# Kernel optimization log

Measured on AMD Instinct MI355X. Metric: run time of the kernel, lower is better.

The kernel has to match this reference:

```python
import jax, jax.numpy as jnp
import numpy as np

VOCAB, E, H = 10000, 128, 256
B, K = 32768, 8


def setup_inputs() -> dict:
    key = jax.random.key(0)
    ks = jax.random.split(key, 14)
    s_in = 1.0 / np.sqrt(E + H)
    return {
        "x": jax.random.randint(ks[0], (1, B), 0, VOCAB),
        "h_pre": jax.random.normal(ks[1], (B, H), jnp.float32),
        "c_pre": jax.random.normal(ks[2], (B, H), jnp.float32),
        "child_cells": jax.random.normal(ks[3], (K, B, H), jnp.float32),
        "child_weights": jax.random.normal(ks[4], (K, B, H), jnp.float32),
        "embed_table": jax.random.normal(ks[5], (VOCAB, E), jnp.float32) * 0.02,
        "Wf": jax.random.normal(ks[6], (H, E + H), jnp.float32) * s_in,
        "bf": jnp.zeros((H,), jnp.float32),
        "Wi": jax.random.normal(ks[7], (H, E + H), jnp.float32) * s_in,
        "bi": jnp.zeros((H,), jnp.float32),
        "Wo": jax.random.normal(ks[8], (H, E + H), jnp.float32) * s_in,
        "bo": jnp.zeros((H,), jnp.float32),
        "Wc": jax.random.normal(ks[9], (H, E + H), jnp.float32) * s_in,
        "bc": jnp.zeros((H,), jnp.float32),
    }


def reference(x, h_pre, c_pre, child_cells, child_weights, embed_table,
              Wf, bf, Wi, bi, Wo, bo, Wc, bc):
    emb = embed_table[x[0]]                      # [B, E]  (squeeze(0))
    xh = jnp.concatenate([emb, h_pre], axis=1)   # [B, E+H] shared concat
    f = jax.nn.sigmoid(xh @ Wf.T + bf)           # [B, H]
    i = jax.nn.sigmoid(xh @ Wi.T + bi)
    c_ = jnp.tanh(xh @ Wc.T + bc)
    # tree-LSTM branch: softmax over [own candidate + K children] along axis 0
    all_cells = jnp.concatenate([c_[None], child_cells], axis=0)      # [K+1,B,H]
    all_w = jnp.concatenate([i[None], child_weights], axis=0)         # [K+1,B,H]
    w = jax.nn.softmax(all_w, axis=0)
    c_cur = jnp.sum(w * all_cells, axis=0)       # [B, H]
    o = jax.nn.sigmoid(xh @ Wo.T + bo)
    h_cur = o * jnp.tanh(c_cur)
    return (h_cur, c_cur)
```

## Files before the change

### kernel.cpp

```cpp
#include <hip/hip_runtime.h>

#define B_SZ   32768
#define H_SZ   256
#define E_SZ   128
#define K_CH   8
#define XH_K   384
#define N_G    768

typedef __attribute__((ext_vector_type(8))) short  short8;
typedef __attribute__((ext_vector_type(4))) short  s16x4;
typedef __attribute__((ext_vector_type(4))) float  f32x4;

static __device__ __forceinline__ short f2bf(float f) {
  union { float f; unsigned u; } v; v.f = f;
  unsigned u = v.u;
  return (short)((u + 0x7fffu + ((u >> 16) & 1u)) >> 16);
}

static __device__ __forceinline__ float bf2f(short s) {
  union { unsigned u; float f; } v;
  v.u = ((unsigned)(unsigned short)s) << 16;
  return v.f;
}

static __device__ __forceinline__ float sigmoid_f(float x) {
  return 1.0f / (1.0f + __expf(-x));
}

static __device__ __forceinline__ float tanh_f(float x) {
  float xc = fminf(fmaxf(x, -40.0f), 40.0f);
  float e  = __expf(2.0f * xc);
  return (e - 1.0f) / (e + 1.0f);
}

static __device__ __forceinline__ f32x4 exp4(f32x4 x) {
  f32x4 r;
#pragma unroll
  for (int c = 0; c < 4; ++c) r[c] = __expf(x[c]);
  return r;
}

static __device__ __forceinline__ void gload_lds16(const short* g, short* l) {
  __builtin_amdgcn_global_load_lds(
      (const __attribute__((address_space(1))) unsigned int*)g,
      (__attribute__((address_space(3))) unsigned int*)l, 16, 0, 0);
}

__global__ __launch_bounds__(256) void prep_xh(const int* __restrict__ x,
                                               const float* __restrict__ h_pre,
                                               const float* __restrict__ emb,
                                               short* __restrict__ xh) {
  int t = blockIdx.x * 256 + threadIdx.x;
  int b = t / 96;
  int c = (t - b * 96) * 4;
  f32x4 v;
  if (c < E_SZ) {
    int row = x[b];
    v = *(const f32x4*)(emb + (size_t)row * E_SZ + c);
  } else {
    v = *(const f32x4*)(h_pre + (size_t)b * H_SZ + (c - E_SZ));
  }
  s16x4 o;
#pragma unroll
  for (int i = 0; i < 4; ++i) o[i] = f2bf(v[i]);
  *(s16x4*)(xh + (size_t)b * XH_K + c) = o;
}

__global__ __launch_bounds__(256) void prep_w(const float* __restrict__ Wi,
                                              const float* __restrict__ Wo,
                                              const float* __restrict__ Wc,
                                              short* __restrict__ Wcat) {
  int t = blockIdx.x * 256 + threadIdx.x;
  int n = t / 96;
  int c = (t - n * 96) * 4;
  const float* src = (n < H_SZ)     ? (Wi + (size_t)n * XH_K)
                   : (n < 2 * H_SZ) ? (Wo + (size_t)(n - H_SZ) * XH_K)
                                    : (Wc + (size_t)(n - 2 * H_SZ) * XH_K);
  f32x4 v = *(const f32x4*)(src + c);
  s16x4 o;
#pragma unroll
  for (int i = 0; i < 4; ++i) o[i] = f2bf(v[i]);
  *(s16x4*)(Wcat + (size_t)n * XH_K + c) = o;
}

__global__ __launch_bounds__(256) void gemm_gates(const short* __restrict__ xh,
                                                  const short* __restrict__ Wcat,
                                                  const float* __restrict__ bi,
                                                  const float* __restrict__ bo,
                                                  const float* __restrict__ bc,
                                                  short* __restrict__ gates) {
  __shared__ short As[128 * 32];
  __shared__ short Bs[128 * 32];

  const int wave = threadIdx.x >> 6;
  const int lane = threadIdx.x & 63;
  const int ln = lane & 15;
  const int q  = lane >> 4;
  const int m0 = blockIdx.y * 128 + (wave >> 1) * 64;
  const int n0 = blockIdx.x * 128 + (wave & 1) * 64;
  const int Am = blockIdx.y * 128;
  const int Bn = blockIdx.x * 128;

  f32x4 acc[4][4] = {};

  for (int ks = 0; ks < 12; ++ks) {
    if (ks) __syncthreads();
#pragma unroll
    for (int s = 0; s < 2; ++s) {
      const int segb = s * 256 + wave * 64;
      const int seg  = segb + lane;
      const int row  = seg >> 2;
      const int ch8  = (seg & 3) * 8;
      gload_lds16(xh   + (size_t)(Am + row) * XH_K + ks * 32 + ch8, &As[segb * 8]);
      gload_lds16(Wcat + (size_t)(Bn + row) * XH_K + ks * 32 + ch8, &Bs[segb * 8]);
    }
    __syncthreads();

    short8 a[4], b[4];
    const int mw = (wave >> 1) * 64;
    const int nw = (wave & 1) * 64;
#pragma unroll
    for (int i = 0; i < 4; ++i)
      a[i] = *(const short8*)&As[(mw + i * 16 + ln) * 32 + q * 8];
#pragma unroll
    for (int j = 0; j < 4; ++j)
      b[j] = *(const short8*)&Bs[(nw + j * 16 + ln) * 32 + q * 8];
#pragma unroll
    for (int i = 0; i < 4; ++i)
#pragma unroll
      for (int j = 0; j < 4; ++j)
        acc[i][j] = __builtin_amdgcn_mfma_f32_16x16x32_bf16(a[i], b[j], acc[i][j], 0, 0, 0);
  }

#pragma unroll
  for (int j = 0; j < 4; ++j) {
    const int col  = n0 + j * 16 + ln;
    const int gate = col >> 8;
    const int cc   = col & 255;
    const float bias = (gate == 0) ? bi[cc] : (gate == 1) ? bo[cc] : bc[cc];
#pragma unroll
    for (int i = 0; i < 4; ++i) {
#pragma unroll
      for (int r = 0; r < 4; ++r) {
        const int row = m0 + i * 16 + q * 4 + r;
        float v = acc[i][j][r] + bias;
        v = (gate == 2) ? tanh_f(v) : sigmoid_f(v);
        gates[(size_t)row * N_G + col] = f2bf(v);
      }
    }
  }
}

__global__ __launch_bounds__(256, 4) void combine(const short* __restrict__ gates,
                                                  const float* __restrict__ ccells,
                                                  const float* __restrict__ cweights,
                                                  float* __restrict__ out) {
  int t = blockIdx.x * 256 + threadIdx.x;
  int b = t >> 5;
  int h = (t & 31) * 8;
  const short* grow = gates + (size_t)b * N_G;

  s16x4 i0 = *(const s16x4*)(grow + h);
  s16x4 i1 = *(const s16x4*)(grow + h + 4);
  s16x4 o0 = *(const s16x4*)(grow + H_SZ + h);
  s16x4 o1 = *(const s16x4*)(grow + H_SZ + h + 4);
  s16x4 c0 = *(const s16x4*)(grow + 2 * H_SZ + h);
  s16x4 c1 = *(const s16x4*)(grow + 2 * H_SZ + h + 4);

  f32x4 iv0, iv1, cv0, cv1;
#pragma unroll
  for (int c = 0; c < 4; ++c) {
    iv0[c] = bf2f(i0[c]); iv1[c] = bf2f(i1[c]);
    cv0[c] = bf2f(c0[c]); cv1[c] = bf2f(c1[c]);
  }

  f32x4 e0 = exp4(iv0), e1 = exp4(iv1);
  f32x4 num0 = e0 * cv0, num1 = e1 * cv1;
  f32x4 den0 = e0,       den1 = e1;

#pragma unroll
  for (int k = 0; k < K_CH; ++k) {
    size_t off = ((size_t)k * B_SZ + b) * H_SZ + h;
    f32x4 w0 = *(const f32x4*)(cweights + off);
    f32x4 w1 = *(const f32x4*)(cweights + off + 4);
    f32x4 l0 = *(const f32x4*)(ccells + off);
    f32x4 l1 = *(const f32x4*)(ccells + off + 4);
    f32x4 x0 = exp4(w0), x1 = exp4(w1);
    num0 += x0 * l0;  den0 += x0;
    num1 += x1 * l1;  den1 += x1;
  }

  f32x4 hv0, hv1, cc0, cc1;
#pragma unroll
  for (int c = 0; c < 4; ++c) {
    cc0[c] = num0[c] / den0[c];
    cc1[c] = num1[c] / den1[c];
    hv0[c] = bf2f(o0[c]) * tanh_f(cc0[c]);
    hv1[c] = bf2f(o1[c]) * tanh_f(cc1[c]);
  }
  float* oh = out + (size_t)b * H_SZ + h;
  float* oc = out + (size_t)B_SZ * H_SZ + (size_t)b * H_SZ + h;
  *(f32x4*)oh = hv0;  *(f32x4*)(oh + 4) = hv1;
  *(f32x4*)oc = cc0;  *(f32x4*)(oc + 4) = cc1;
}

extern "C" void kernel_launch(void* const* d_in, const int* in_sizes, int n_in,
                              void* d_out, int out_size, void* d_ws, size_t ws_size,
                              hipStream_t stream) {
  const int*   x             = (const int*)d_in[0];
  const float* h_pre         = (const float*)d_in[1];
  const float* child_cells   = (const float*)d_in[3];
  const float* child_weights = (const float*)d_in[4];
  const float* emb           = (const float*)d_in[5];
  const float* Wi            = (const float*)d_in[8];
  const float* bi            = (const float*)d_in[9];
  const float* Wo            = (const float*)d_in[10];
  const float* bo            = (const float*)d_in[11];
  const float* Wc            = (const float*)d_in[12];
  const float* bc            = (const float*)d_in[13];
  float* out = (float*)d_out;

  char* ws = (char*)d_ws;
  short* xh    = (short*)ws;
  short* Wcat  = (short*)(ws + (size_t)B_SZ * XH_K * 2);
  short* gates = (short*)(ws + (size_t)B_SZ * XH_K * 2
                             + (size_t)N_G * XH_K * 2);

  prep_xh<<<dim3(B_SZ * 96 / 256), dim3(256), 0, stream>>>(x, h_pre, emb, xh);
  prep_w <<<dim3(N_G * 96 / 256),  dim3(256), 0, stream>>>(Wi, Wo, Wc, Wcat);
  gemm_gates<<<dim3(6, 256), dim3(256), 0, stream>>>(xh, Wcat, bi, bo, bc, gates);
  combine<<<dim3(B_SZ * 32 / 256), dim3(256), 0, stream>>>(gates, child_cells, child_weights, out);
}
```

Baseline: 648.8 us.

## Widen GEMM K-tile with XOR-swizzled LDS and batch child loads in combine

The gate GEMM now stages 64-wide K slices, which halves the number of barrier-separated iterations. It stores them in LDS with an XOR swizzle on 16-byte chunks to avoid bank conflicts on the MFMA operand reads. The combine kernel now handles 4 elements per thread instead of 8, doubling the thread count, and issues all 16 child loads before any arithmetic to expose more memory-level parallelism. It also drops the occupancy hint from launch bounds. The trade-off is more LDS per block and more registers held per thread for the batched loads.

```diff
diff --git a/kernel.cpp b/kernel.cpp
--- a/kernel.cpp
+++ b/kernel.cpp
@@ -31,13 +31,6 @@
   float xc = fminf(fmaxf(x, -40.0f), 40.0f);
   float e  = __expf(2.0f * xc);
   return (e - 1.0f) / (e + 1.0f);
-}
-
-static __device__ __forceinline__ f32x4 exp4(f32x4 x) {
-  f32x4 r;
-#pragma unroll
-  for (int c = 0; c < 4; ++c) r[c] = __expf(x[c]);
-  return r;
 }
 
 static __device__ __forceinline__ void gload_lds16(const short* g, short* l) {
@@ -89,8 +82,8 @@
                                                   const float* __restrict__ bo,
                                                   const float* __restrict__ bc,
                                                   short* __restrict__ gates) {
-  __shared__ short As[128 * 32];
-  __shared__ short Bs[128 * 32];
+  __shared__ short As[128 * 64];
+  __shared__ short Bs[128 * 64];
 
   const int wave = threadIdx.x >> 6;
   const int lane = threadIdx.x & 63;
@@ -103,33 +96,42 @@
 
   f32x4 acc[4][4] = {};
 
-  for (int ks = 0; ks < 12; ++ks) {
+  for (int ks = 0; ks < 6; ++ks) {
     if (ks) __syncthreads();
 #pragma unroll
-    for (int s = 0; s < 2; ++s) {
+    for (int s = 0; s < 4; ++s) {
       const int segb = s * 256 + wave * 64;
       const int seg  = segb + lane;
-      const int row  = seg >> 2;
-      const int ch8  = (seg & 3) * 8;
-      gload_lds16(xh   + (size_t)(Am + row) * XH_K + ks * 32 + ch8, &As[segb * 8]);
-      gload_lds16(Wcat + (size_t)(Bn + row) * XH_K + ks * 32 + ch8, &Bs[segb * 8]);
+      const int row  = seg >> 3;
+      const int ch8  = ((seg & 7) ^ (row & 7)) * 8;
+      gload_lds16(xh   + (size_t)(Am + row) * XH_K + ks * 64 + ch8, &As[segb * 8]);
+      gload_lds16(Wcat + (size_t)(Bn + row) * XH_K + ks * 64 + ch8, &Bs[segb * 8]);
     }
     __syncthreads();
 
-    short8 a[4], b[4];
+    short8 a[2][4], b[2][4];
     const int mw = (wave >> 1) * 64;
     const int nw = (wave & 1) * 64;
 #pragma unroll
-    for (int i = 0; i < 4; ++i)
-      a[i] = *(const short8*)&As[(mw + i * 16 + ln) * 32 + q * 8];
-#pragma unroll
-    for (int j = 0; j < 4; ++j)
-      b[j] = *(const short8*)&Bs[(nw + j * 16 + ln) * 32 + q * 8];
-#pragma unroll
-    for (int i = 0; i < 4; ++i)
-#pragma unroll
-      for (int j = 0; j < 4; ++j)
-        acc[i][j] = __builtin_amdgcn_mfma_f32_16x16x32_bf16(a[i], b[j], acc[i][j], 0, 0, 0);
+    for (int kk = 0; kk < 2; ++kk) {
+#pragma unroll
+      for (int i = 0; i < 4; ++i) {
+        const int r = mw + i * 16 + ln;
+        a[kk][i] = *(const short8*)&As[r * 64 + (((kk * 4 + q) ^ (r & 7)) * 8)];
+      }
+#pragma unroll
+      for (int j = 0; j < 4; ++j) {
+        const int r = nw + j * 16 + ln;
+        b[kk][j] = *(const short8*)&Bs[r * 64 + (((kk * 4 + q) ^ (r & 7)) * 8)];
+      }
+    }
+#pragma unroll
+    for (int kk = 0; kk < 2; ++kk)
+#pragma unroll
+      for (int i = 0; i < 4; ++i)
+#pragma unroll
+        for (int j = 0; j < 4; ++j)
+          acc[i][j] = __builtin_amdgcn_mfma_f32_16x16x32_bf16(a[kk][i], b[kk][j], acc[i][j], 0, 0, 0);
   }
 
 #pragma unroll
@@ -151,57 +153,54 @@
   }
 }
 
-__global__ __launch_bounds__(256, 4) void combine(const short* __restrict__ gates,
-                                                  const float* __restrict__ ccells,
-                                                  const float* __restrict__ cweights,
-                                                  float* __restrict__ out) {
+__global__ __launch_bounds__(256) void combine(const short* __restrict__ gates,
+                                               const float* __restrict__ ccells,
+                                               const float* __restrict__ cweights,
+                                               float* __restrict__ out) {
   int t = blockIdx.x * 256 + threadIdx.x;
-  int b = t >> 5;
-  int h = (t & 31) * 8;
+  int b = t >> 6;
+  int h = (t & 63) * 4;
   const short* grow = gates + (size_t)b * N_G;
 
-  s16x4 i0 = *(const s16x4*)(grow + h);
-  s16x4 i1 = *(const s16x4*)(grow + h + 4);
-  s16x4 o0 = *(const s16x4*)(grow + H_SZ + h);
-  s16x4 o1 = *(const s16x4*)(grow + H_SZ + h + 4);
-  s16x4 c0 = *(const s16x4*)(grow + 2 * H_SZ + h);
-  s16x4 c1 = *(const s16x4*)(grow + 2 * H_SZ + h + 4);
-
-  f32x4 iv0, iv1, cv0, cv1;
-#pragma unroll
-  for (int c = 0; c < 4; ++c) {
-    iv0[c] = bf2f(i0[c]); iv1[c] = bf2f(i1[c]);
-    cv0[c] = bf2f(c0[c]); cv1[c] = bf2f(c1[c]);
-  }
-
-  f32x4 e0 = exp4(iv0), e1 = exp4(iv1);
-  f32x4 num0 = e0 * cv0, num1 = e1 * cv1;
-  f32x4 den0 = e0,       den1 = e1;
-
+  f32x4 w[K_CH], l[K_CH];
 #pragma unroll
   for (int k = 0; k < K_CH; ++k) {
     size_t off = ((size_t)k * B_SZ + b) * H_SZ + h;
-    f32x4 w0 = *(const f32x4*)(cweights + off);
-    f32x4 w1 = *(const f32x4*)(cweights + off + 4);
-    f32x4 l0 = *(const f32x4*)(ccells + off);
-    f32x4 l1 = *(const f32x4*)(ccells + off + 4);
-    f32x4 x0 = exp4(w0), x1 = exp4(w1);
-    num0 += x0 * l0;  den0 += x0;
-    num1 += x1 * l1;  den1 += x1;
-  }
-
-  f32x4 hv0, hv1, cc0, cc1;
+    w[k] = *(const f32x4*)(cweights + off);
+    l[k] = *(const f32x4*)(ccells + off);
+  }
+  s16x4 ig = *(const s16x4*)(grow + h);
+  s16x4 og = *(const s16x4*)(grow + H_SZ + h);
+  s16x4 cg = *(const s16x4*)(grow + 2 * H_SZ + h);
+
+  f32x4 num, den;
 #pragma unroll
   for (int c = 0; c < 4; ++c) {
-    cc0[c] = num0[c] / den0[c];
-    cc1[c] = num1[c] / den1[c];
-    hv0[c] = bf2f(o0[c]) * tanh_f(cc0[c]);
-    hv1[c] = bf2f(o1[c]) * tanh_f(cc1[c]);
+    float e = __expf(bf2f(ig[c]));
+    num[c] = e * bf2f(cg[c]);
+    den[c] = e;
+  }
+
+#pragma unroll
+  for (int k = 0; k < K_CH; ++k) {
+#pragma unroll
+    for (int c = 0; c < 4; ++c) {
+      float e = __expf(w[k][c]);
+      num[c] += e * l[k][c];
+      den[c] += e;
+    }
+  }
+
+  f32x4 hv, cc;
+#pragma unroll
+  for (int c = 0; c < 4; ++c) {
+    cc[c] = num[c] / den[c];
+    hv[c] = bf2f(og[c]) * tanh_f(cc[c]);
   }
   float* oh = out + (size_t)b * H_SZ + h;
   float* oc = out + (size_t)B_SZ * H_SZ + (size_t)b * H_SZ + h;
-  *(f32x4*)oh = hv0;  *(f32x4*)(oh + 4) = hv1;
-  *(f32x4*)oc = cc0;  *(f32x4*)(oc + 4) = cc1;
+  *(f32x4*)oh = hv;
+  *(f32x4*)oc = cc;
 }
 
 extern "C" void kernel_launch(void* const* d_in, const int* in_sizes, int n_in,
@@ -229,5 +228,5 @@
   prep_xh<<<dim3(B_SZ * 96 / 256), dim3(256), 0, stream>>>(x, h_pre, emb, xh);
   prep_w <<<dim3(N_G * 96 / 256),  dim3(256), 0, stream>>>(Wi, Wo, Wc, Wcat);
   gemm_gates<<<dim3(6, 256), dim3(256), 0, stream>>>(xh, Wcat, bi, bo, bc, gates);
-  combine<<<dim3(B_SZ * 32 / 256), dim3(256), 0, stream>>>(gates, child_cells, child_weights, out);
-}
+  combine<<<dim3(B_SZ * 64 / 256), dim3(256), 0, stream>>>(gates, child_cells, child_weights, out);
+}
```

New measurement: 652.9 us. No clear change (+0.6%).
